# Kernel tuning notes

Measured on AMD Instinct MI355X. Metric: run time of the kernel, lower is better.

## Reference

```python
import jax, jax.numpy as jnp
import numpy as np

B, C, H, W = 4, 128, 192, 192

def _conv(x, w, b, pad):
    y = jax.lax.conv_general_dilated(
        x, w, window_strides=(1, 1), padding=[(pad, pad), (pad, pad)],
        dimension_numbers=('NCHW', 'OIHW', 'NCHW'))
    return y + b[None, :, None, None]

def setup_inputs() -> dict:
    key = jax.random.key(0)
    ks = jax.random.split(key, 11)
    def he(k, shape):
        fan_in = shape[1] * shape[2] * shape[3]
        return jax.random.normal(k, shape, jnp.float32) * np.sqrt(2.0 / fan_in)
    return {
        'x':  jax.random.normal(ks[0], (B, C, H, W), jnp.float32),
        'w1': he(ks[1], (C // 2, C, 3, 3)),      'b1': jnp.zeros((C // 2,), jnp.float32),
        'w2': he(ks[2], (C // 4, C // 2, 3, 3)), 'b2': jnp.zeros((C // 4,), jnp.float32),
        'w3': he(ks[3], (9, C // 4, 1, 1)),      'b3': jnp.zeros((9,), jnp.float32),
        'f1': he(ks[4], (C, C, 3, 3)),           'fb1': jnp.zeros((C,), jnp.float32),
        'f2': he(ks[5], (C, C, 3, 3)),           'fb2': jnp.zeros((C,), jnp.float32),
    }

def reference(x, w1, b1, w2, b2, w3, b3, f1, fb1, f2, fb2):
    b, c, h, w = x.shape
    # kernel estimator: conv3x3 -> relu -> conv3x3 -> relu -> conv1x1 (9 logits)
    k = jax.nn.relu(_conv(x, w1, b1, 1))
    k = jax.nn.relu(_conv(k, w2, b2, 1))
    k = _conv(k, w3, b3, 0)                     # (b, 9, h, w)
    kernel = jax.nn.softmax(k, axis=1)[:, None]  # (b, 1, 9, h, w)
    # 3x3 neighborhoods (equivalent to F.unfold with padding=1), row-major taps
    xp = jnp.pad(x, ((0, 0), (0, 0), (1, 1), (1, 1)))
    patches = jnp.stack([xp[:, :, i:i + h, j:j + w]
                         for i in range(3) for j in range(3)], axis=2)  # (b, c, 9, h, w)
    out = jnp.sum(patches * kernel, axis=2)     # (b, c, h, w)
    # feature extract
    feats = jax.nn.relu(_conv(out, f1, fb1, 1))
    feats = _conv(feats, f2, fb2, 1)
    return feats
```

## Files before the change

kernel.cpp:

```cpp
#include <hip/hip_runtime.h>
#include <math.h>

#define BB 4
#define CC 128
#define HH 192
#define WW 192
#define HWSZ (HH * WW)
#define NPIX (BB * HWSZ)
#define PD 194

typedef __attribute__((ext_vector_type(8))) short short8;
typedef __attribute__((ext_vector_type(4))) short short4v;
typedef __attribute__((ext_vector_type(4))) float float4v;

__device__ __forceinline__ short f2bf(float f) {
    unsigned u = __float_as_uint(f);
    u += 0x7FFF + ((u >> 16) & 1);
    return (short)(u >> 16);
}
__device__ __forceinline__ float bf2f(short s) {
    return __uint_as_float(((unsigned)(unsigned short)s) << 16);
}

__global__ void prep_w_kernel(const float* __restrict__ w,
                              short* __restrict__ wp,
                              int CIN, int COUT, int NSLICE, int total) {
    int idx = blockIdx.x * blockDim.x + threadIdx.x;
    if (idx >= total) return;
    int CKN = CIN / 32;
    int ci8 = idx & 7;
    int t   = idx >> 3;
    int co  = t % COUT;  t /= COUT;
    int lg  = t % 4;     t /= 4;
    int tap3 = t % 3;    t /= 3;
    int tt  = t % 3;     t /= 3;
    int ck  = t % CKN;
    int sl  = t / CKN;
    int cin = ck * 32 + lg * 8 + ci8;
    int tap = tt * 3 + tap3;
    int co_g = sl * COUT + co;
    wp[idx] = f2bf(w[(co_g * CIN + cin) * 9 + tap]);
}

__global__ void zero_pads_kernel(short* __restrict__ p0,
                                 short* __restrict__ p1,
                                 short* __restrict__ p2) {
    int idx = blockIdx.x * blockDim.x + threadIdx.x;
    if (idx >= 3 * 64 * 772) return;
    int e   = idx % 772;
    int bc  = (idx / 772) % 64;
    int buf = idx / (772 * 64);
    short* base = (buf == 0) ? p0 : (buf == 1) ? p1 : p2;
    int row, col;
    if (e < 194)      { row = 0;   col = e; }
    else if (e < 388) { row = 193; col = e - 194; }
    else { int e2 = e - 388; row = 1 + (e2 >> 1); col = (e2 & 1) * 193; }
    short8 z = {0, 0, 0, 0, 0, 0, 0, 0};
    *(short8*)&base[(((size_t)bc * PD + row) * PD + col) * 8] = z;
}

__global__ void x_prep_kernel(const float* __restrict__ x,
                              short* __restrict__ xp) {
    int idx = blockIdx.x * blockDim.x + threadIdx.x;
    if (idx >= BB * 16 * HWSZ) return;
    int w  = idx % WW;
    int h  = (idx / WW) % HH;
    int cg = (idx / HWSZ) % 16;
    int b  = idx / (HWSZ * 16);
    const float* p = x + ((size_t)(b * CC + cg * 8) * HH + h) * WW + w;
    short8 pk;
#pragma unroll
    for (int j = 0; j < 8; ++j) pk[j] = f2bf(p[(size_t)j * HWSZ]);
    *(short8*)&xp[((((size_t)b * 16 + cg) * PD + h + 1) * PD + (w + 1)) * 8] = pk;
}

template <int CIN, int COUT, int NSLICE, int WAVES_M, int WAVES_N, int WM, int WN,
          bool RELU, bool OUT_F32>
__global__ __launch_bounds__(WAVES_M * WAVES_N * 64, 4)
void conv3x3_wlds(const short* __restrict__ in,
                  const short* __restrict__ wp,
                  const float* __restrict__ bias,
                  void* __restrict__ outv) {
    constexpr int CKN   = CIN / 32;
    constexpr int CG_IN = CIN / 8;
    constexpr int COUT_TOT = COUT * NSLICE;
    constexpr int CGO   = COUT_TOT / 8;
    constexpr int NT    = WAVES_M * WAVES_N * 64;
    constexpr int SUB   = 3 * 4 * COUT * 8;
    constexpr int SUBB  = SUB * 2;
    constexpr int ATS   = 4 * COUT * 16;
    constexpr int NS    = CKN * 3;
    constexpr int KTMAX = CKN * 9;
    constexpr int CKB   = PD * PD * 64;
    constexpr int WPSL  = NS * SUB;
    constexpr int NWG   = BB * HH * NSLICE;
    static_assert(WAVES_M * WM * 16 == COUT, "M tiling");
    static_assert(WAVES_N * WN * 16 == 192, "N tiling");

    __shared__ __align__(16) short s_w[2 * SUB];

    const int tid  = threadIdx.x;
    const int lin  = blockIdx.y * (HH * NSLICE) + blockIdx.x;
    const int L    = (lin & 7) * (NWG >> 3) + (lin >> 3);
    const int sl   = L % NSLICE;
    const int h    = (L / NSLICE) % HH;
    const int b    = L / (NSLICE * HH);
    const int lane = tid & 63;
    const int wv   = tid >> 6;
    const int wv_m = wv % WAVES_M;
    const int wv_n = wv / WAVES_M;
    const int ln15 = lane & 15;
    const int lg   = lane >> 4;

    float4v acc[WM][WN];
#pragma unroll
    for (int mi = 0; mi < WM; ++mi)
#pragma unroll
        for (int ni = 0; ni < WN; ++ni)
            acc[mi][ni] = (float4v){0.f, 0.f, 0.f, 0.f};

    short8 Aa[2][WM], Bb[3][WN];

    const int colb = (wv_n * WN * 16 + ln15) * 16;
    const char* rowb0 = (const char*)(in +
        (((size_t)b * CG_IN + lg) * PD + h) * (size_t)PD * 8) + colb;
    const char* rowb1 = rowb0 + PD * 16;
    const char* rowb2 = rowb0 + 2 * PD * 16;

    const char* aBase = (const char*)&s_w[0] +
        lg * (COUT * 16) + (wv_m * WM) * 256 + ln15 * 16;

    auto loadBpf = [&](int dy, int dx, short8* dst) {
        const char* rp = (dy == 0) ? rowb0 : (dy == 1) ? rowb1 : rowb2;
#pragma unroll
        for (int ni = 0; ni < WN; ++ni)
            dst[ni] = *(const short8*)(rp + dx * 16 + ni * 256);
    };

    const short* wsrc = wp + (size_t)sl * WPSL;
    int wpar = 0;
    auto stageIssue = [&]() {
        constexpr int UNITS = SUB / 8;
        short* dstb = &s_w[wpar * SUB];
#pragma unroll
        for (int u = 0; u < (UNITS + NT - 1) / NT; ++u) {
            int i = tid + u * NT;
            if (UNITS % NT == 0 || i < UNITS)
                __builtin_amdgcn_global_load_lds(
                    (const __attribute__((address_space(1))) void*)&wsrc[i * 8],
                    (__attribute__((address_space(3))) void*)&dstb[i * 8], 16, 0, 0);
        }
        asm volatile("" ::: "memory");
        wsrc += SUB;
        wpar ^= 1;
    };

    stageIssue();
    loadBpf(0, 0, Bb[0]);
    loadBpf(0, 1, Bb[1]);
    asm volatile("s_waitcnt vmcnt(6)" ::: "memory");
    __builtin_amdgcn_s_barrier();
    asm volatile("" ::: "memory");

    int par = 0;
    for (int ck = 0; ck < CKN; ++ck) {
#pragma unroll
        for (int tt = 0; tt < 3; ++tt) {
            const int s = ck * 3 + tt;
            const bool notLast = (s + 1 < NS);
            if (notLast) stageIssue();
            const char* aP = aBase + (par ? SUBB : 0);
#pragma unroll
            for (int mi = 0; mi < WM; ++mi)
                Aa[0][mi] = *(const short8*)(aP + mi * 256);
#pragma unroll
            for (int t3 = 0; t3 < 3; ++t3) {
                if (t3 < 2) {
#pragma unroll
                    for (int mi = 0; mi < WM; ++mi)
                        Aa[(t3 + 1) & 1][mi] =
                            *(const short8*)(aP + (t3 + 1) * ATS + mi * 256);
                }
                const int kt = s * 3 + t3;
                if (kt + 2 < KTMAX) {
                    const int tp = (tt * 3 + t3 + 2) % 9;
                    loadBpf(tp / 3, tp % 3, Bb[(t3 + 2) % 3]);
                }
                __builtin_amdgcn_s_setprio(1);
#pragma unroll
                for (int mi = 0; mi < WM; ++mi)
#pragma unroll
                    for (int ni = 0; ni < WN; ++ni)
                        acc[mi][ni] = __builtin_amdgcn_mfma_f32_16x16x32_bf16(
                            Aa[t3 & 1][mi], Bb[t3][ni], acc[mi][ni], 0, 0, 0);
                __builtin_amdgcn_s_setprio(0);
                if (tt == 2 && t3 == 0) {
                    rowb0 += CKB; rowb1 += CKB; rowb2 += CKB;
                }
            }
            if (notLast) {
                asm volatile("s_waitcnt vmcnt(9)" ::: "memory");
                __builtin_amdgcn_s_barrier();
                asm volatile("" ::: "memory");
                par ^= 1;
            }
        }
    }

    if (OUT_F32) {
        float* out = (float*)outv;
#pragma unroll
        for (int mi = 0; mi < WM; ++mi) {
            int co0 = sl * COUT + (wv_m * WM + mi) * 16 + lg * 4;
#pragma unroll
            for (int r = 0; r < 4; ++r) {
                int co = co0 + r;
                float bv = bias[co];
#pragma unroll
                for (int ni = 0; ni < WN; ++ni) {
                    int wcol = (wv_n * WN + ni) * 16 + ln15;
                    float v = acc[mi][ni][r] + bv;
                    if (RELU) v = fmaxf(v, 0.f);
                    out[((size_t)(b * COUT_TOT + co) * HH + h) * WW + wcol] = v;
                }
            }
        }
    } else {
        short* out = (short*)outv;
#pragma unroll
        for (int mi = 0; mi < WM; ++mi) {
            int co0 = sl * COUT + (wv_m * WM + mi) * 16 + lg * 4;
            int cg  = co0 >> 3;
            int sub = co0 & 7;
#pragma unroll
            for (int ni = 0; ni < WN; ++ni) {
                int wcol = (wv_n * WN + ni) * 16 + ln15;
                short4v pk;
#pragma unroll
                for (int r = 0; r < 4; ++r) {
                    float v = acc[mi][ni][r] + bias[co0 + r];
                    if (RELU) v = fmaxf(v, 0.f);
                    pk[r] = f2bf(v);
                }
                *(short4v*)&out[((((size_t)b * CGO + cg) * PD + (h + 1)) * PD +
                                 (wcol + 1)) * 8 + sub] = pk;
            }
        }
    }
}

__global__ void conv1x1_softmax_kernel(const short* __restrict__ t2,
                                       const float* __restrict__ w3,
                                       const float* __restrict__ b3,
                                       float* __restrict__ kern) {
    __shared__ float sw[9 * 32];
    __shared__ float sb[9];
    for (int i = threadIdx.x; i < 9 * 32; i += blockDim.x) sw[i] = w3[i];
    if (threadIdx.x < 9) sb[threadIdx.x] = b3[threadIdx.x];
    __syncthreads();

    int idx = blockIdx.x * blockDim.x + threadIdx.x;
    if (idx >= NPIX) return;
    int b = idx / HWSZ;
    int p = idx % HWSZ;
    int h = p / WW, w = p % WW;

    float v[32];
#pragma unroll
    for (int cg = 0; cg < 4; ++cg) {
        short8 pk = *(const short8*)
            &t2[((((size_t)b * 4 + cg) * PD + h + 1) * PD + (w + 1)) * 8];
#pragma unroll
        for (int j = 0; j < 8; ++j) v[cg * 8 + j] = bf2f(pk[j]);
    }

    float lg[9];
    float m = -1e30f;
#pragma unroll
    for (int t = 0; t < 9; ++t) {
        float s = sb[t];
#pragma unroll
        for (int c = 0; c < 32; ++c) s = fmaf(sw[t * 32 + c], v[c], s);
        lg[t] = s;
        m = fmaxf(m, s);
    }
    float sum = 0.f;
#pragma unroll
    for (int t = 0; t < 9; ++t) {
        lg[t] = __expf(lg[t] - m);
        sum += lg[t];
    }
    float inv = 1.f / sum;
#pragma unroll
    for (int t = 0; t < 9; ++t)
        kern[((size_t)(b * 9 + t)) * HWSZ + p] = lg[t] * inv;
}

__global__ void deblur_kernel(const float* __restrict__ x,
                              const float* __restrict__ kern,
                              short* __restrict__ t3) {
    int idx = blockIdx.x * blockDim.x + threadIdx.x;
    if (idx >= BB * 16 * HWSZ) return;
    int w  = idx % WW;
    int h  = (idx / WW) % HH;
    int cg = (idx / HWSZ) % 16;
    int b  = idx / (HWSZ * 16);

    const float* kb = kern + (size_t)(b * 9) * HWSZ + h * WW + w;
    float kv[9];
#pragma unroll
    for (int t = 0; t < 9; ++t) kv[t] = kb[(size_t)t * HWSZ];

    const float* xb = x + (size_t)(b * CC + cg * 8) * HWSZ;
    float s[8] = {0.f, 0.f, 0.f, 0.f, 0.f, 0.f, 0.f, 0.f};
    int t = 0;
#pragma unroll
    for (int dy = 0; dy < 3; ++dy) {
#pragma unroll
        for (int dx = 0; dx < 3; ++dx) {
            int hh = h + dy - 1, ww2 = w + dx - 1;
            if ((unsigned)hh < (unsigned)HH && (unsigned)ww2 < (unsigned)WW) {
                const float* xp = xb + hh * WW + ww2;
#pragma unroll
                for (int j = 0; j < 8; ++j)
                    s[j] = fmaf(kv[t], xp[(size_t)j * HWSZ], s[j]);
            }
            ++t;
        }
    }
    short8 pk;
#pragma unroll
    for (int j = 0; j < 8; ++j) pk[j] = f2bf(s[j]);
    *(short8*)&t3[((((size_t)b * 16 + cg) * PD + h + 1) * PD + (w + 1)) * 8] = pk;
}

extern "C" void kernel_launch(void* const* d_in, const int* in_sizes, int n_in,
                              void* d_out, int out_size, void* d_ws, size_t ws_size,
                              hipStream_t stream) {
    const float* x   = (const float*)d_in[0];
    const float* w1  = (const float*)d_in[1];
    const float* b1  = (const float*)d_in[2];
    const float* w2  = (const float*)d_in[3];
    const float* b2  = (const float*)d_in[4];
    const float* w3  = (const float*)d_in[5];
    const float* b3  = (const float*)d_in[6];
    const float* f1  = (const float*)d_in[7];
    const float* fb1 = (const float*)d_in[8];
    const float* f2  = (const float*)d_in[9];
    const float* fb2 = (const float*)d_in[10];
    float* out = (float*)d_out;

    const size_t ACT_SZ = (size_t)BB * 16 * PD * PD * 8;
    short* xpad    = (short*)d_ws;
    short* regionA = xpad + ACT_SZ;
    short* regionB = regionA + ACT_SZ;
    float* kern    = (float*)(regionB + ACT_SZ);
    short* wp1     = (short*)(kern + (size_t)BB * 9 * HWSZ);
    short* wp2     = wp1 + 9 * 4 * 64 * 32;
    short* wpf1    = wp2 + 9 * 2 * 32 * 32;
    short* wpf2    = wpf1 + 9 * 4 * 128 * 32;

    short* t1 = regionA;
    short* t2 = regionB;
    short* t3 = regionA;
    short* t4 = regionB;

    {
        int nz = 3 * 64 * 772;
        zero_pads_kernel<<<(nz + 255) / 256, 256, 0, stream>>>(xpad, regionA, regionB);
        int nx = BB * 16 * HWSZ;
        x_prep_kernel<<<(nx + 255) / 256, 256, 0, stream>>>(x, xpad);
        int n1 = 9 * 4 * 64 * 32, n2 = 9 * 2 * 32 * 32, nf = 9 * 4 * 128 * 32;
        prep_w_kernel<<<(n1 + 255) / 256, 256, 0, stream>>>(w1, wp1, 128, 64, 1, n1);
        prep_w_kernel<<<(n2 + 255) / 256, 256, 0, stream>>>(w2, wp2, 64, 32, 1, n2);
        prep_w_kernel<<<(nf + 255) / 256, 256, 0, stream>>>(f1, wpf1, 128, 64, 2, nf);
        prep_w_kernel<<<(nf + 255) / 256, 256, 0, stream>>>(f2, wpf2, 128, 64, 2, nf);
    }

    conv3x3_wlds<128, 64, 1, 1, 4, 4, 3, true, false>
        <<<dim3(HH, BB), 256, 0, stream>>>(xpad, wp1, b1, t1);
    conv3x3_wlds<64, 32, 1, 1, 4, 2, 3, true, false>
        <<<dim3(HH, BB), 256, 0, stream>>>(t1, wp2, b2, t2);
    conv1x1_softmax_kernel<<<(NPIX + 255) / 256, 256, 0, stream>>>(t2, w3, b3, kern);
    {
        int nd = BB * 16 * HWSZ;
        deblur_kernel<<<(nd + 255) / 256, 256, 0, stream>>>(x, kern, t3);
    }
    conv3x3_wlds<128, 64, 2, 1, 4, 4, 3, true, false>
        <<<dim3(HH * 2, BB), 256, 0, stream>>>(t3, wpf1, fb1, t4);
    conv3x3_wlds<128, 64, 2, 1, 4, 4, 3, false, true>
        <<<dim3(HH * 2, BB), 256, 0, stream>>>(t4, wpf2, fb2, out);
}
```

Measured before the change: 330.2 us.

## Switch conv3x3 to 32x32x16 MFMA with six waves per row

```diff
diff --git a/kernel.cpp b/kernel.cpp
--- a/kernel.cpp
+++ b/kernel.cpp
@@ -11,7 +11,7 @@
 
 typedef __attribute__((ext_vector_type(8))) short short8;
 typedef __attribute__((ext_vector_type(4))) short short4v;
-typedef __attribute__((ext_vector_type(4))) float float4v;
+typedef __attribute__((ext_vector_type(16))) float float16v;
 
 __device__ __forceinline__ short f2bf(float f) {
     unsigned u = __float_as_uint(f);
@@ -31,12 +31,13 @@
     int ci8 = idx & 7;
     int t   = idx >> 3;
     int co  = t % COUT;  t /= COUT;
-    int lg  = t % 4;     t /= 4;
+    int hi  = t % 2;     t /= 2;
+    int kh  = t % 2;     t /= 2;
     int tap3 = t % 3;    t /= 3;
     int tt  = t % 3;     t /= 3;
     int ck  = t % CKN;
     int sl  = t / CKN;
-    int cin = ck * 32 + lg * 8 + ci8;
+    int cin = ck * 32 + (kh * 2 + hi) * 8 + ci8;
     int tap = tt * 3 + tap3;
     int co_g = sl * COUT + co;
     wp[idx] = f2bf(w[(co_g * CIN + cin) * 9 + tap]);
@@ -74,9 +75,8 @@
     *(short8*)&xp[((((size_t)b * 16 + cg) * PD + h + 1) * PD + (w + 1)) * 8] = pk;
 }
 
-template <int CIN, int COUT, int NSLICE, int WAVES_M, int WAVES_N, int WM, int WN,
-          bool RELU, bool OUT_F32>
-__global__ __launch_bounds__(WAVES_M * WAVES_N * 64, 4)
+template <int CIN, int COUT, int NSLICE, int WM, bool RELU, bool OUT_F32>
+__global__ __launch_bounds__(384, 3)
 void conv3x3_wlds(const short* __restrict__ in,
                   const short* __restrict__ wp,
                   const float* __restrict__ bias,
@@ -85,17 +85,18 @@
     constexpr int CG_IN = CIN / 8;
     constexpr int COUT_TOT = COUT * NSLICE;
     constexpr int CGO   = COUT_TOT / 8;
-    constexpr int NT    = WAVES_M * WAVES_N * 64;
-    constexpr int SUB   = 3 * 4 * COUT * 8;
+    constexpr int NT    = 384;
+    constexpr int SUB   = 3 * 2 * 2 * COUT * 8;
     constexpr int SUBB  = SUB * 2;
-    constexpr int ATS   = 4 * COUT * 16;
+    constexpr int A_T3  = 4 * COUT * 16;
+    constexpr int A_KH  = 2 * COUT * 16;
     constexpr int NS    = CKN * 3;
     constexpr int KTMAX = CKN * 9;
     constexpr int CKB   = PD * PD * 64;
     constexpr int WPSL  = NS * SUB;
     constexpr int NWG   = BB * HH * NSLICE;
-    static_assert(WAVES_M * WM * 16 == COUT, "M tiling");
-    static_assert(WAVES_N * WN * 16 == 192, "N tiling");
+    static_assert(WM * 32 == COUT, "M tiling");
+    static_assert((SUB / 8) % NT == 0, "DMA units divide thread count");
 
     __shared__ __align__(16) short s_w[2 * SUB];
 
@@ -107,34 +108,34 @@
     const int b    = L / (NSLICE * HH);
     const int lane = tid & 63;
     const int wv   = tid >> 6;
-    const int wv_m = wv % WAVES_M;
-    const int wv_n = wv / WAVES_M;
-    const int ln15 = lane & 15;
-    const int lg   = lane >> 4;
-
-    float4v acc[WM][WN];
+    const int l31  = lane & 31;
+    const int hi   = lane >> 5;
+
+    float16v acc[WM];
 #pragma unroll
     for (int mi = 0; mi < WM; ++mi)
 #pragma unroll
-        for (int ni = 0; ni < WN; ++ni)
-            acc[mi][ni] = (float4v){0.f, 0.f, 0.f, 0.f};
-
-    short8 Aa[2][WM], Bb[3][WN];
-
-    const int colb = (wv_n * WN * 16 + ln15) * 16;
-    const char* rowb0 = (const char*)(in +
-        (((size_t)b * CG_IN + lg) * PD + h) * (size_t)PD * 8) + colb;
-    const char* rowb1 = rowb0 + PD * 16;
-    const char* rowb2 = rowb0 + 2 * PD * 16;
-
-    const char* aBase = (const char*)&s_w[0] +
-        lg * (COUT * 16) + (wv_m * WM) * 256 + ln15 * 16;
-
-    auto loadBpf = [&](int dy, int dx, short8* dst) {
-        const char* rp = (dy == 0) ? rowb0 : (dy == 1) ? rowb1 : rowb2;
-#pragma unroll
-        for (int ni = 0; ni < WN; ++ni)
-            dst[ni] = *(const short8*)(rp + dx * 16 + ni * 256);
+        for (int e = 0; e < 16; ++e) acc[mi][e] = 0.f;
+
+    short8 Aa[2][2][WM];
+    short8 Bb[3][2];
+
+    const int colb = (wv * 32 + l31) * 16;
+    const char* r00 = (const char*)in +
+        ((((size_t)b * CG_IN + hi) * PD + h) * PD) * 16 + colb;
+    const char* r01 = r00 + (size_t)2 * PD * PD * 16;
+    const char* r10 = r00 + PD * 16;
+    const char* r11 = r01 + PD * 16;
+    const char* r20 = r00 + 2 * PD * 16;
+    const char* r21 = r01 + 2 * PD * 16;
+
+    const char* aBase = (const char*)&s_w[0] + (hi * COUT + l31) * 16;
+
+    auto loadB = [&](int dy, int dx, int slot) {
+        const char* p0 = (dy == 0) ? r00 : (dy == 1) ? r10 : r20;
+        const char* p1 = (dy == 0) ? r01 : (dy == 1) ? r11 : r21;
+        Bb[slot][0] = *(const short8*)(p0 + dx * 16);
+        Bb[slot][1] = *(const short8*)(p1 + dx * 16);
     };
 
     const short* wsrc = wp + (size_t)sl * WPSL;
@@ -143,12 +144,11 @@
         constexpr int UNITS = SUB / 8;
         short* dstb = &s_w[wpar * SUB];
 #pragma unroll
-        for (int u = 0; u < (UNITS + NT - 1) / NT; ++u) {
+        for (int u = 0; u < UNITS / NT; ++u) {
             int i = tid + u * NT;
-            if (UNITS % NT == 0 || i < UNITS)
-                __builtin_amdgcn_global_load_lds(
-                    (const __attribute__((address_space(1))) void*)&wsrc[i * 8],
-                    (__attribute__((address_space(3))) void*)&dstb[i * 8], 16, 0, 0);
+            __builtin_amdgcn_global_load_lds(
+                (const __attribute__((address_space(1))) void*)&wsrc[i * 8],
+                (__attribute__((address_space(3))) void*)&dstb[i * 8], 16, 0, 0);
         }
         asm volatile("" ::: "memory");
         wsrc += SUB;
@@ -156,9 +156,9 @@
     };
 
     stageIssue();
-    loadBpf(0, 0, Bb[0]);
-    loadBpf(0, 1, Bb[1]);
-    asm volatile("s_waitcnt vmcnt(6)" ::: "memory");
+    loadB(0, 0, 0);
+    loadB(0, 1, 1);
+    asm volatile("s_waitcnt vmcnt(4)" ::: "memory");
     __builtin_amdgcn_s_barrier();
     asm volatile("" ::: "memory");
 
@@ -171,35 +171,41 @@
             if (notLast) stageIssue();
             const char* aP = aBase + (par ? SUBB : 0);
 #pragma unroll
-            for (int mi = 0; mi < WM; ++mi)
-                Aa[0][mi] = *(const short8*)(aP + mi * 256);
+            for (int kh = 0; kh < 2; ++kh)
+#pragma unroll
+                for (int mi = 0; mi < WM; ++mi)
+                    Aa[0][kh][mi] = *(const short8*)
+                        (aP + kh * A_KH + mi * 512);
 #pragma unroll
             for (int t3 = 0; t3 < 3; ++t3) {
                 if (t3 < 2) {
 #pragma unroll
-                    for (int mi = 0; mi < WM; ++mi)
-                        Aa[(t3 + 1) & 1][mi] =
-                            *(const short8*)(aP + (t3 + 1) * ATS + mi * 256);
+                    for (int kh = 0; kh < 2; ++kh)
+#pragma unroll
+                        for (int mi = 0; mi < WM; ++mi)
+                            Aa[(t3 + 1) & 1][kh][mi] = *(const short8*)
+                                (aP + (t3 + 1) * A_T3 + kh * A_KH + mi * 512);
                 }
                 const int kt = s * 3 + t3;
                 if (kt + 2 < KTMAX) {
                     const int tp = (tt * 3 + t3 + 2) % 9;
-                    loadBpf(tp / 3, tp % 3, Bb[(t3 + 2) % 3]);
+                    loadB(tp / 3, tp % 3, (t3 + 2) % 3);
                 }
                 __builtin_amdgcn_s_setprio(1);
 #pragma unroll
                 for (int mi = 0; mi < WM; ++mi)
 #pragma unroll
-                    for (int ni = 0; ni < WN; ++ni)
-                        acc[mi][ni] = __builtin_amdgcn_mfma_f32_16x16x32_bf16(
-                            Aa[t3 & 1][mi], Bb[t3][ni], acc[mi][ni], 0, 0, 0);
+                    for (int kh = 0; kh < 2; ++kh)
+                        acc[mi] = __builtin_amdgcn_mfma_f32_32x32x16_bf16(
+                            Aa[t3 & 1][kh][mi], Bb[t3][kh], acc[mi], 0, 0, 0);
                 __builtin_amdgcn_s_setprio(0);
                 if (tt == 2 && t3 == 0) {
-                    rowb0 += CKB; rowb1 += CKB; rowb2 += CKB;
+                    r00 += CKB; r01 += CKB; r10 += CKB;
+                    r11 += CKB; r20 += CKB; r21 += CKB;
                 }
             }
             if (notLast) {
-                asm volatile("s_waitcnt vmcnt(9)" ::: "memory");
+                asm volatile("s_waitcnt vmcnt(4)" ::: "memory");
                 __builtin_amdgcn_s_barrier();
                 asm volatile("" ::: "memory");
                 par ^= 1;
@@ -207,21 +213,20 @@
         }
     }
 
+    const int px = wv * 32 + l31;
     if (OUT_F32) {
         float* out = (float*)outv;
 #pragma unroll
         for (int mi = 0; mi < WM; ++mi) {
-            int co0 = sl * COUT + (wv_m * WM + mi) * 16 + lg * 4;
-#pragma unroll
-            for (int r = 0; r < 4; ++r) {
-                int co = co0 + r;
-                float bv = bias[co];
-#pragma unroll
-                for (int ni = 0; ni < WN; ++ni) {
-                    int wcol = (wv_n * WN + ni) * 16 + ln15;
-                    float v = acc[mi][ni][r] + bv;
+#pragma unroll
+            for (int q = 0; q < 4; ++q) {
+                int co0 = sl * COUT + mi * 32 + q * 8 + hi * 4;
+#pragma unroll
+                for (int e = 0; e < 4; ++e) {
+                    int co = co0 + e;
+                    float v = acc[mi][q * 4 + e] + bias[co];
                     if (RELU) v = fmaxf(v, 0.f);
-                    out[((size_t)(b * COUT_TOT + co) * HH + h) * WW + wcol] = v;
+                    out[((size_t)(b * COUT_TOT + co) * HH + h) * WW + px] = v;
                 }
             }
         }
@@ -229,21 +234,20 @@
         short* out = (short*)outv;
 #pragma unroll
         for (int mi = 0; mi < WM; ++mi) {
-            int co0 = sl * COUT + (wv_m * WM + mi) * 16 + lg * 4;
-            int cg  = co0 >> 3;
-            int sub = co0 & 7;
-#pragma unroll
-            for (int ni = 0; ni < WN; ++ni) {
-                int wcol = (wv_n * WN + ni) * 16 + ln15;
+#pragma unroll
+            for (int q = 0; q < 4; ++q) {
+                int co0 = sl * COUT + mi * 32 + q * 8 + hi * 4;
+                int cg  = co0 >> 3;
+                int sub = co0 & 7;
                 short4v pk;
 #pragma unroll
-                for (int r = 0; r < 4; ++r) {
-                    float v = acc[mi][ni][r] + bias[co0 + r];
+                for (int e = 0; e < 4; ++e) {
+                    float v = acc[mi][q * 4 + e] + bias[co0 + e];
                     if (RELU) v = fmaxf(v, 0.f);
-                    pk[r] = f2bf(v);
+                    pk[e] = f2bf(v);
                 }
                 *(short4v*)&out[((((size_t)b * CGO + cg) * PD + (h + 1)) * PD +
-                                 (wcol + 1)) * 8 + sub] = pk;
+                                 (px + 1)) * 8 + sub] = pk;
             }
         }
     }
@@ -377,17 +381,17 @@
         prep_w_kernel<<<(nf + 255) / 256, 256, 0, stream>>>(f2, wpf2, 128, 64, 2, nf);
     }
 
-    conv3x3_wlds<128, 64, 1, 1, 4, 4, 3, true, false>
-        <<<dim3(HH, BB), 256, 0, stream>>>(xpad, wp1, b1, t1);
-    conv3x3_wlds<64, 32, 1, 1, 4, 2, 3, true, false>
-        <<<dim3(HH, BB), 256, 0, stream>>>(t1, wp2, b2, t2);
+    conv3x3_wlds<128, 64, 1, 2, true, false>
+        <<<dim3(HH, BB), 384, 0, stream>>>(xpad, wp1, b1, t1);
+    conv3x3_wlds<64, 32, 1, 1, true, false>
+        <<<dim3(HH, BB), 384, 0, stream>>>(t1, wp2, b2, t2);
     conv1x1_softmax_kernel<<<(NPIX + 255) / 256, 256, 0, stream>>>(t2, w3, b3, kern);
     {
         int nd = BB * 16 * HWSZ;
         deblur_kernel<<<(nd + 255) / 256, 256, 0, stream>>>(x, kern, t3);
     }
-    conv3x3_wlds<128, 64, 2, 1, 4, 4, 3, true, false>
-        <<<dim3(HH * 2, BB), 256, 0, stream>>>(t3, wpf1, fb1, t4);
-    conv3x3_wlds<128, 64, 2, 1, 4, 4, 3, false, true>
-        <<<dim3(HH * 2, BB), 256, 0, stream>>>(t4, wpf2, fb2, out);
-}
+    conv3x3_wlds<128, 64, 2, 2, true, false>
+        <<<dim3(HH * 2, BB), 384, 0, stream>>>(t3, wpf1, fb1, t4);
+    conv3x3_wlds<128, 64, 2, 2, false, true>
+        <<<dim3(HH * 2, BB), 384, 0, stream>>>(t4, wpf2, fb2, out);
+}
```

New measurement: 349.0 us. +5.7%, slower.

## Fuse 1x1 conv softmax into deblur and split first conv across output groups

Applied to the files above, without the earlier changes.

```diff
diff --git a/kernel.cpp b/kernel.cpp
--- a/kernel.cpp
+++ b/kernel.cpp
@@ -249,10 +249,11 @@
     }
 }
 
-__global__ void conv1x1_softmax_kernel(const short* __restrict__ t2,
-                                       const float* __restrict__ w3,
-                                       const float* __restrict__ b3,
-                                       float* __restrict__ kern) {
+__global__ void softmax_deblur_kernel(const short* __restrict__ t2,
+                                      const float* __restrict__ w3,
+                                      const float* __restrict__ b3,
+                                      const float* __restrict__ x,
+                                      short* __restrict__ t3) {
     __shared__ float sw[9 * 32];
     __shared__ float sb[9];
     for (int i = threadIdx.x; i < 9 * 32; i += blockDim.x) sw[i] = w3[i];
@@ -260,9 +261,11 @@
     __syncthreads();
 
     int idx = blockIdx.x * blockDim.x + threadIdx.x;
-    if (idx >= NPIX) return;
-    int b = idx / HWSZ;
-    int p = idx % HWSZ;
+    if (idx >= 4 * NPIX) return;
+    int qc  = idx / NPIX;
+    int pid = idx % NPIX;
+    int b = pid / HWSZ;
+    int p = pid % HWSZ;
     int h = p / WW, w = p % WW;
 
     float v[32];
@@ -273,65 +276,51 @@
 #pragma unroll
         for (int j = 0; j < 8; ++j) v[cg * 8 + j] = bf2f(pk[j]);
     }
-
-    float lg[9];
+    float kv[9];
     float m = -1e30f;
 #pragma unroll
     for (int t = 0; t < 9; ++t) {
         float s = sb[t];
 #pragma unroll
         for (int c = 0; c < 32; ++c) s = fmaf(sw[t * 32 + c], v[c], s);
-        lg[t] = s;
+        kv[t] = s;
         m = fmaxf(m, s);
     }
     float sum = 0.f;
 #pragma unroll
     for (int t = 0; t < 9; ++t) {
-        lg[t] = __expf(lg[t] - m);
-        sum += lg[t];
+        kv[t] = __expf(kv[t] - m);
+        sum += kv[t];
     }
     float inv = 1.f / sum;
 #pragma unroll
-    for (int t = 0; t < 9; ++t)
-        kern[((size_t)(b * 9 + t)) * HWSZ + p] = lg[t] * inv;
-}
-
-__global__ void deblur_kernel(const float* __restrict__ x,
-                              const float* __restrict__ kern,
-                              short* __restrict__ t3) {
-    int idx = blockIdx.x * blockDim.x + threadIdx.x;
-    if (idx >= BB * 16 * HWSZ) return;
-    int w  = idx % WW;
-    int h  = (idx / WW) % HH;
-    int cg = (idx / HWSZ) % 16;
-    int b  = idx / (HWSZ * 16);
-
-    const float* kb = kern + (size_t)(b * 9) * HWSZ + h * WW + w;
-    float kv[9];
-#pragma unroll
-    for (int t = 0; t < 9; ++t) kv[t] = kb[(size_t)t * HWSZ];
-
-    const float* xb = x + (size_t)(b * CC + cg * 8) * HWSZ;
-    float s[8] = {0.f, 0.f, 0.f, 0.f, 0.f, 0.f, 0.f, 0.f};
-    int t = 0;
-#pragma unroll
-    for (int dy = 0; dy < 3; ++dy) {
-#pragma unroll
-        for (int dx = 0; dx < 3; ++dx) {
-            int hh = h + dy - 1, ww2 = w + dx - 1;
-            if ((unsigned)hh < (unsigned)HH && (unsigned)ww2 < (unsigned)WW) {
-                const float* xp = xb + hh * WW + ww2;
-#pragma unroll
-                for (int j = 0; j < 8; ++j)
-                    s[j] = fmaf(kv[t], xp[(size_t)j * HWSZ], s[j]);
-            }
-            ++t;
-        }
-    }
-    short8 pk;
-#pragma unroll
-    for (int j = 0; j < 8; ++j) pk[j] = f2bf(s[j]);
-    *(short8*)&t3[((((size_t)b * 16 + cg) * PD + h + 1) * PD + (w + 1)) * 8] = pk;
+    for (int t = 0; t < 9; ++t) kv[t] *= inv;
+
+#pragma unroll
+    for (int cgo = 0; cgo < 4; ++cgo) {
+        int cg = qc * 4 + cgo;
+        const float* xb = x + (size_t)(b * CC + cg * 8) * HWSZ;
+        float s[8] = {0.f, 0.f, 0.f, 0.f, 0.f, 0.f, 0.f, 0.f};
+        int t = 0;
+#pragma unroll
+        for (int dy = 0; dy < 3; ++dy) {
+#pragma unroll
+            for (int dx = 0; dx < 3; ++dx) {
+                int hh = h + dy - 1, ww2 = w + dx - 1;
+                if ((unsigned)hh < (unsigned)HH && (unsigned)ww2 < (unsigned)WW) {
+                    const float* xp = xb + hh * WW + ww2;
+#pragma unroll
+                    for (int j = 0; j < 8; ++j)
+                        s[j] = fmaf(kv[t], xp[(size_t)j * HWSZ], s[j]);
+                }
+                ++t;
+            }
+        }
+        short8 pk;
+#pragma unroll
+        for (int j = 0; j < 8; ++j) pk[j] = f2bf(s[j]);
+        *(short8*)&t3[((((size_t)b * 16 + cg) * PD + h + 1) * PD + (w + 1)) * 8] = pk;
+    }
 }
 
 extern "C" void kernel_launch(void* const* d_in, const int* in_sizes, int n_in,
@@ -371,21 +360,18 @@
         int nx = BB * 16 * HWSZ;
         x_prep_kernel<<<(nx + 255) / 256, 256, 0, stream>>>(x, xpad);
         int n1 = 9 * 4 * 64 * 32, n2 = 9 * 2 * 32 * 32, nf = 9 * 4 * 128 * 32;
-        prep_w_kernel<<<(n1 + 255) / 256, 256, 0, stream>>>(w1, wp1, 128, 64, 1, n1);
+        prep_w_kernel<<<(n1 + 255) / 256, 256, 0, stream>>>(w1, wp1, 128, 32, 2, n1);
         prep_w_kernel<<<(n2 + 255) / 256, 256, 0, stream>>>(w2, wp2, 64, 32, 1, n2);
         prep_w_kernel<<<(nf + 255) / 256, 256, 0, stream>>>(f1, wpf1, 128, 64, 2, nf);
         prep_w_kernel<<<(nf + 255) / 256, 256, 0, stream>>>(f2, wpf2, 128, 64, 2, nf);
     }
 
-    conv3x3_wlds<128, 64, 1, 1, 4, 4, 3, true, false>
-        <<<dim3(HH, BB), 256, 0, stream>>>(xpad, wp1, b1, t1);
+    conv3x3_wlds<128, 32, 2, 1, 4, 2, 3, true, false>
+        <<<dim3(HH * 2, BB), 256, 0, stream>>>(xpad, wp1, b1, t1);
     conv3x3_wlds<64, 32, 1, 1, 4, 2, 3, true, false>
         <<<dim3(HH, BB), 256, 0, stream>>>(t1, wp2, b2, t2);
-    conv1x1_softmax_kernel<<<(NPIX + 255) / 256, 256, 0, stream>>>(t2, w3, b3, kern);
-    {
-        int nd = BB * 16 * HWSZ;
-        deblur_kernel<<<(nd + 255) / 256, 256, 0, stream>>>(x, kern, t3);
-    }
+    softmax_deblur_kernel<<<(4 * NPIX + 255) / 256, 256, 0, stream>>>(
+        t2, w3, b3, x, t3);
     conv3x3_wlds<128, 64, 2, 1, 4, 4, 3, true, false>
         <<<dim3(HH * 2, BB), 256, 0, stream>>>(t3, wpf1, fb1, t4);
     conv3x3_wlds<128, 64, 2, 1, 4, 4, 3, false, true>
```

After: 333.9 us. No clear change (+1.1%).
